# Kernel optimization log

Hardware: AMD Instinct MI355X
Metric: run time of the kernel (lower is better)

The kernel has to match this reference:

```python
import jax, jax.numpy as jnp
import numpy as np

C = 768      # token feature dim
N = 196      # tokens per stream
R_DIM = 2 * 2 * N  # 784 = concat(A row, A col)


def setup_inputs() -> dict:
    key = jax.random.key(0)
    ks = jax.random.split(key, 16)
    s = 1.0 / np.sqrt(C)
    inp = {
        "x": jax.random.normal(ks[0], (128, N, C), dtype=jnp.float32),
        "y": jax.random.normal(ks[1], (128, N, C), dtype=jnp.float32),
        # linear_conv_1: 1x1 conv (768->768) + BN affine (eval) + ReLU
        "W1": jax.random.normal(ks[2], (C, C), dtype=jnp.float32) * s,
        "b1": jnp.zeros((C,), dtype=jnp.float32),
        "g1": jax.random.uniform(ks[3], (C,), dtype=jnp.float32, minval=0.5, maxval=1.5),
        "be1": jax.random.normal(ks[4], (C,), dtype=jnp.float32) * 0.1,
        # linear_conv_2
        "W2": jax.random.normal(ks[5], (C, C), dtype=jnp.float32) * s,
        "b2": jnp.zeros((C,), dtype=jnp.float32),
        "g2": jax.random.uniform(ks[6], (C,), dtype=jnp.float32, minval=0.5, maxval=1.5),
        "be2": jax.random.normal(ks[7], (C,), dtype=jnp.float32) * 0.1,
        # linear_conv_3: 768->768
        "W3": jax.random.normal(ks[8], (C, C), dtype=jnp.float32) * s,
        "b3": jnp.zeros((C,), dtype=jnp.float32),
        # linear_conv_4: 784->784 over relation rows
        "W4": jax.random.normal(ks[9], (784, 784), dtype=jnp.float32) / np.sqrt(784.0),
        "b4": jnp.zeros((784,), dtype=jnp.float32),
        # linear_conv_5: (768+784)->1
        "W5": jax.random.normal(ks[10], (C + 784, 1), dtype=jnp.float32) / np.sqrt(C + 784.0),
        "b5": jnp.zeros((1,), dtype=jnp.float32),
    }
    return inp


def reference(x, y, W1, b1, g1, be1, W2, b2, g2, be2, W3, b3, W4, b4, W5, b5):
    # per-token 1x1 conv + BN(eval)->affine + ReLU
    phi_x = jax.nn.relu((x @ W1 + b1) * g1 + be1)          # [B,196,768]
    phi_y = jax.nn.relu((y @ W2 + b2) * g2 + be2)          # [B,196,768]
    cat_phi = jnp.concatenate([phi_x, phi_y], axis=1)      # [B,392,768]
    # affinity matrix A = cat_phi @ cat_phi^T
    A = jnp.einsum("bnd,bmd->bnm", cat_phi, cat_phi)       # [B,392,392]
    # R[i] = concat(A[i,:], A[:,i]) -> vectorized as [A | A^T]
    R = jnp.concatenate([A, jnp.swapaxes(A, 1, 2)], axis=2)  # [B,392,784]
    v = cat_phi @ W3 + b3                                   # [B,392,768]
    v_ = R @ W4 + b4                                        # [B,392,784]
    cat_v = jnp.concatenate([v, v_], axis=2)                # [B,392,1552]
    W = cat_v @ W5 + b5                                     # [B,392,1]
    # per-token reweighting then sum of the two streams
    out = x * W[:, :N, :] + y * W[:, N:, :]                 # [B,196,768]
    return out
```

## Files before the change

### kernel.cpp

```cpp
#include <hip/hip_runtime.h>

typedef __bf16 bf16_t;
typedef bf16_t bf16x8 __attribute__((ext_vector_type(8)));
typedef float f32x4 __attribute__((ext_vector_type(4)));
typedef unsigned short u16x8 __attribute__((ext_vector_type(8)));
typedef unsigned short u16x4 __attribute__((ext_vector_type(4)));

#define CD 768
#define NT 196
#define NB 128
#define T2 392
#define MROWS (NB*NT)

__device__ __forceinline__ unsigned short f2bf(float f){
  unsigned u = __float_as_uint(f);
  u += 0x7fffu + ((u >> 16) & 1u);
  return (unsigned short)(u >> 16);
}
__device__ __forceinline__ float bf2f(unsigned short h){
  return __uint_as_float(((unsigned)h) << 16);
}
__device__ __forceinline__ float wave_reduce(float v){
  #pragma unroll
  for (int o = 32; o > 0; o >>= 1) v += __shfl_down(v, o, 64);
  return v;
}
__device__ __forceinline__ void gload16(const unsigned short* g, unsigned short* l){
  __builtin_amdgcn_global_load_lds(
      (const __attribute__((address_space(1))) unsigned int*)g,
      (__attribute__((address_space(3))) unsigned int*)l, 16, 0, 0);
}

__global__ __launch_bounds__(256) void prep_wt(const float* __restrict__ W1,
                        const float* __restrict__ W2,
                        unsigned short* __restrict__ W1t, unsigned short* __restrict__ W2t){
  __shared__ float tile[64][65];
  const float* src = blockIdx.z ? W2 : W1;
  unsigned short* dst = blockIdx.z ? W2t : W1t;
  int k0 = blockIdx.x*64, n0 = blockIdx.y*64;
  int tid = threadIdx.x;
  #pragma unroll
  for (int e = 0; e < 16; ++e){
    int idx = e*256 + tid;
    int r = idx >> 6, c = idx & 63;
    tile[r][c] = src[(size_t)(k0+r)*CD + n0 + c];
  }
  __syncthreads();
  #pragma unroll
  for (int e = 0; e < 16; ++e){
    int idx = e*256 + tid;
    int nr = idx >> 6, kc = idx & 63;
    dst[(size_t)(n0+nr)*CD + k0 + kc] = f2bf(tile[kc][nr]);
  }
}

__global__ void prep_u(const float* __restrict__ W3, const float* __restrict__ W4,
                       const float* __restrict__ W5, const float* __restrict__ b3,
                       const float* __restrict__ b4, const float* __restrict__ b5,
                       float* __restrict__ u3, float* __restrict__ u4s, float* __restrict__ cbuf){
  int wid = (blockIdx.x*blockDim.x + threadIdx.x) >> 6;
  int lane = threadIdx.x & 63;
  const float* w5a = W5;
  const float* w5b = W5 + CD;
  float s = 0.f;
  if (wid < CD){
    const float* row = W3 + (size_t)wid*CD;
    for (int k = lane; k < CD; k += 64) s += row[k]*w5a[k];
    s = wave_reduce(s);
    if (lane == 0) u3[wid] = s;
  } else if (wid < CD + T2){
    int j = wid - CD;
    const float* r0 = W4 + (size_t)j*784;
    const float* r1 = W4 + (size_t)(j+T2)*784;
    for (int e = lane; e < 784; e += 64) s += (r0[e]+r1[e])*w5b[e];
    s = wave_reduce(s);
    if (lane == 0) u4s[j] = s;
  } else if (wid == CD + T2){
    for (int k = lane; k < CD; k += 64) s += b3[k]*w5a[k];
    for (int e = lane; e < 784; e += 64) s += b4[e]*w5b[e];
    s = wave_reduce(s);
    if (lane == 0) cbuf[0] = s + b5[0];
  }
}

__global__ void init_t(const float* __restrict__ u3, float* __restrict__ t){
  int i = blockIdx.x*256 + threadIdx.x;
  if (i < (NB+1)*CD) t[i] = (i < NB*CD) ? u3[i % CD] : 0.f;
}

__global__ __launch_bounds__(256) void cvt2(const float* __restrict__ x,
                                            const float* __restrict__ y,
                                            unsigned short* __restrict__ dst){
  const int nv = MROWS*CD/8;
  for (int id = blockIdx.x*256 + threadIdx.x; id < 2*nv; id += gridDim.x*256){
    const float* s = (id < nv) ? x : y;
    int i = (id < nv) ? id : id - nv;
    float4 a = ((const float4*)s)[i*2];
    float4 b = ((const float4*)s)[i*2+1];
    u16x8 o = { f2bf(a.x), f2bf(a.y), f2bf(a.z), f2bf(a.w),
                f2bf(b.x), f2bf(b.y), f2bf(b.z), f2bf(b.w) };
    ((u16x8*)dst)[id] = o;
  }
}

__global__ __launch_bounds__(256, 2) void phi_gemm(
    const unsigned short* __restrict__ A, const unsigned short* __restrict__ Bt,
    const float* __restrict__ bias, const float* __restrict__ gam,
    const float* __restrict__ bet, const float* __restrict__ u4c,
    unsigned short* __restrict__ phi, float* __restrict__ t)
{
  __shared__ unsigned short As[2][128*64];
  __shared__ unsigned short Bs[2][128*64];

  const int tid  = threadIdx.x;
  const int lane = tid & 63;
  const int w    = tid >> 6;
  const int wr = w >> 1, wc = w & 1;

  int orig = blockIdx.x;
  int swz  = (orig & 7)*147 + (orig >> 3);
  int bn = swz % 6;
  int bm = swz / 6;

  const int srow = lane >> 3;
  const int p    = lane & 7;
  const int g0   = (p - srow) & 7;
  const unsigned short* a0 = A  + (size_t)(bm*128 + w*32 + srow)*CD + g0*8;
  const unsigned short* b0 = Bt + (size_t)(bn*128 + w*32 + srow)*CD + g0*8;
  unsigned short* al0 = &As[0][w*2048]; unsigned short* bl0 = &Bs[0][w*2048];
  unsigned short* al1 = &As[1][w*2048]; unsigned short* bl1 = &Bs[1][w*2048];

  const int fr = lane & 15, f = lane >> 4, r7 = lane & 7;
  f32x4 acc[4][4] = {};

#define STAGE(AL, BL, KT) { const int ko = (KT)*64;         \
    _Pragma("unroll")                                       \
    for (int c = 0; c < 4; ++c){                            \
      gload16(a0 + (size_t)c*8*CD + ko, AL + c*512);        \
      gload16(b0 + (size_t)c*8*CD + ko, BL + c*512); } }

#define COMPUTE(D) {                                                     \
    _Pragma("unroll")                                                    \
    for (int kk = 0; kk < 2; ++kk){                                      \
      bf16x8 af[4], bq[4];                                               \
      _Pragma("unroll")                                                  \
      for (int mi = 0; mi < 4; ++mi){ int rr = wr*64 + mi*16 + fr;       \
        af[mi] = *(const bf16x8*)(&As[D][rr*64 + (((kk*4+f)+r7)&7)*8]); }\
      _Pragma("unroll")                                                  \
      for (int ni = 0; ni < 4; ++ni){ int cc = wc*64 + ni*16 + fr;       \
        bq[ni] = *(const bf16x8*)(&Bs[D][cc*64 + (((kk*4+f)+r7)&7)*8]); }\
      _Pragma("unroll")                                                  \
      for (int mi = 0; mi < 4; ++mi)                                     \
        _Pragma("unroll")                                                \
        for (int ni = 0; ni < 4; ++ni)                                   \
          acc[mi][ni] = __builtin_amdgcn_mfma_f32_16x16x32_bf16(af[mi], bq[ni], acc[mi][ni], 0, 0, 0); } }

  STAGE(al0, bl0, 0)
  __syncthreads();
  #pragma unroll 1
  for (int kp = 0; kp < 5; ++kp){
    STAGE(al1, bl1, 2*kp+1)
    COMPUTE(0)
    __syncthreads();
    STAGE(al0, bl0, 2*kp+2)
    COMPUTE(1)
    __syncthreads();
  }
  STAGE(al1, bl1, 11)
  COMPUTE(0)
  __syncthreads();
  COMPUTE(1)
#undef COMPUTE
#undef STAGE

  const int b_base = (bm*128) / NT;
  #pragma unroll
  for (int ni = 0; ni < 4; ++ni){
    int col = bn*128 + wc*64 + ni*16 + fr;
    float bi = bias[col], ga = gam[col], be = bet[col];
    float c0 = 0.f, c1 = 0.f;
    #pragma unroll
    for (int mi = 0; mi < 4; ++mi){
      int r0 = bm*128 + wr*64 + mi*16 + f*4;
      #pragma unroll
      for (int j = 0; j < 4; ++j){
        int r = r0 + j;
        float v = fmaxf((acc[mi][ni][j] + bi)*ga + be, 0.f);
        phi[(size_t)r*CD + col] = f2bf(v);
        int b = r / NT;
        int tok = r - b*NT;
        float pv = u4c[tok]*v;
        if (b == b_base) c0 += pv; else c1 += pv;
      }
    }
    c0 += __shfl_xor(c0, 16, 64); c0 += __shfl_xor(c0, 32, 64);
    c1 += __shfl_xor(c1, 16, 64); c1 += __shfl_xor(c1, 32, 64);
    if (lane < 16){
      atomicAdd(&t[(size_t)b_base*CD + col], c0);
      atomicAdd(&t[(size_t)(b_base+1)*CD + col], c1);
    }
  }
}

__global__ __launch_bounds__(256) void comp_wout(
    const unsigned short* __restrict__ phiX, const unsigned short* __restrict__ phiY,
    const float* __restrict__ t, const float* __restrict__ cbuf,
    const float* __restrict__ x, const float* __restrict__ y, float* __restrict__ out)
{
  int gw   = (blockIdx.x*256 + threadIdx.x) >> 6;
  int lane = threadIdx.x & 63;
  int b = gw / NT;
  const unsigned short* px = phiX + (size_t)gw*CD;
  const unsigned short* py = phiY + (size_t)gw*CD;
  const float* tb = t + (size_t)b*CD;
  float s1 = 0.f, s2 = 0.f;
  #pragma unroll
  for (int it = 0; it < 3; ++it){
    int k = it*256 + lane*4;
    float4 tv = *(const float4*)(tb + k);
    u16x4 ux = *(const u16x4*)(px + k);
    u16x4 uy = *(const u16x4*)(py + k);
    s1 += bf2f(ux.x)*tv.x + bf2f(ux.y)*tv.y + bf2f(ux.z)*tv.z + bf2f(ux.w)*tv.w;
    s2 += bf2f(uy.x)*tv.x + bf2f(uy.y)*tv.y + bf2f(uy.z)*tv.z + bf2f(uy.w)*tv.w;
  }
  s1 = wave_reduce(s1);
  s2 = wave_reduce(s2);
  float c = cbuf[0];
  float wx = __shfl(s1, 0, 64) + c;
  float wy = __shfl(s2, 0, 64) + c;
  const float* xr = x + (size_t)gw*CD;
  const float* yr = y + (size_t)gw*CD;
  float* orow = out + (size_t)gw*CD;
  #pragma unroll
  for (int it = 0; it < 3; ++it){
    int k = it*256 + lane*4;
    float4 xv = *(const float4*)(xr + k);
    float4 yv = *(const float4*)(yr + k);
    float4 o;
    o.x = xv.x*wx + yv.x*wy;
    o.y = xv.y*wx + yv.y*wy;
    o.z = xv.z*wx + yv.z*wy;
    o.w = xv.w*wx + yv.w*wy;
    *(float4*)(orow + k) = o;
  }
}

extern "C" void kernel_launch(void* const* d_in, const int* in_sizes, int n_in,
                              void* d_out, int out_size, void* d_ws, size_t ws_size,
                              hipStream_t stream){
  const float* x  = (const float*)d_in[0];
  const float* y  = (const float*)d_in[1];
  const float* W1 = (const float*)d_in[2];
  const float* b1 = (const float*)d_in[3];
  const float* g1 = (const float*)d_in[4];
  const float* be1= (const float*)d_in[5];
  const float* W2 = (const float*)d_in[6];
  const float* b2 = (const float*)d_in[7];
  const float* g2 = (const float*)d_in[8];
  const float* be2= (const float*)d_in[9];
  const float* W3 = (const float*)d_in[10];
  const float* b3 = (const float*)d_in[11];
  const float* W4 = (const float*)d_in[12];
  const float* b4 = (const float*)d_in[13];
  const float* W5 = (const float*)d_in[14];
  const float* b5 = (const float*)d_in[15];
  float* out = (float*)d_out;

  unsigned short* W1t = (unsigned short*)d_ws;
  unsigned short* W2t = W1t + CD*CD;
  unsigned short* S0  = W2t + CD*CD;
  unsigned short* S2  = S0 + (size_t)MROWS*CD;
  unsigned short* S1  = S2 + (size_t)MROWS*CD;
  float* u3   = (float*)(S1 + (size_t)MROWS*CD);
  float* u4s  = u3 + CD;
  float* cbuf = u4s + T2;
  float* t    = cbuf + 4;

  prep_wt<<<dim3(12,12,2), 256, 0, stream>>>(W1, W2, W1t, W2t);
  prep_u<<<(CD + T2 + 4)/4, 256, 0, stream>>>(W3, W4, W5, b3, b4, b5, u3, u4s, cbuf);
  init_t<<<((NB+1)*CD + 255)/256, 256, 0, stream>>>(u3, t);

  cvt2<<<2048, 256, 0, stream>>>(x, y, S0);

  phi_gemm<<<1176, 256, 0, stream>>>(S0, W1t, b1, g1, be1, u4s,      S1, t);
  phi_gemm<<<1176, 256, 0, stream>>>(S2, W2t, b2, g2, be2, u4s + NT, S0, t);

  comp_wout<<<MROWS/4, 256, 0, stream>>>(S1, S0, t, cbuf, x, y, out);
}
```

Measured before the change: 215.6 us.

## Make phi GEMM persistent with cross-tile prefetch and read bf16 inputs in output pass

```diff
diff --git a/kernel.cpp b/kernel.cpp
--- a/kernel.cpp
+++ b/kernel.cpp
@@ -109,35 +109,33 @@
     const float* __restrict__ bet, const float* __restrict__ u4c,
     unsigned short* __restrict__ phi, float* __restrict__ t)
 {
-  __shared__ unsigned short As[2][128*64];
-  __shared__ unsigned short Bs[2][128*64];
+  __shared__ unsigned short As[2][8192];
+  __shared__ unsigned short Bs[2][8192];
 
   const int tid  = threadIdx.x;
   const int lane = tid & 63;
   const int w    = tid >> 6;
   const int wr = w >> 1, wc = w & 1;
 
-  int orig = blockIdx.x;
-  int swz  = (orig & 7)*147 + (orig >> 3);
-  int bn = swz % 6;
-  int bm = swz / 6;
-
   const int srow = lane >> 3;
   const int p    = lane & 7;
   const int g0   = (p - srow) & 7;
-  const unsigned short* a0 = A  + (size_t)(bm*128 + w*32 + srow)*CD + g0*8;
-  const unsigned short* b0 = Bt + (size_t)(bn*128 + w*32 + srow)*CD + g0*8;
-  unsigned short* al0 = &As[0][w*2048]; unsigned short* bl0 = &Bs[0][w*2048];
-  unsigned short* al1 = &As[1][w*2048]; unsigned short* bl1 = &Bs[1][w*2048];
-
+  const size_t arow = (size_t)(w*32 + srow)*CD + g0*8;
   const int fr = lane & 15, f = lane >> 4, r7 = lane & 7;
-  f32x4 acc[4][4] = {};
-
-#define STAGE(AL, BL, KT) { const int ko = (KT)*64;         \
-    _Pragma("unroll")                                       \
-    for (int c = 0; c < 4; ++c){                            \
-      gload16(a0 + (size_t)c*8*CD + ko, AL + c*512);        \
-      gload16(b0 + (size_t)c*8*CD + ko, BL + c*512); } }
+
+  const int x   = blockIdx.x & 7;
+  const int idx = blockIdx.x >> 3;
+  int c  = idx;
+  int g  = x*147 + c;
+  int bm = g/6, bn = g - 6*(g/6);
+  const unsigned short* aP = A  + (size_t)bm*128*CD + arow;
+  const unsigned short* bP = Bt + (size_t)bn*128*CD + arow;
+
+#define STAGE(D, AG, BG, KT) { const int ko = (KT)*64;                  \
+    _Pragma("unroll")                                                   \
+    for (int cc = 0; cc < 4; ++cc){                                     \
+      gload16(AG + (size_t)cc*8*CD + ko, &As[D][w*2048 + cc*512]);      \
+      gload16(BG + (size_t)cc*8*CD + ko, &Bs[D][w*2048 + cc*512]); } }
 
 #define COMPUTE(D) {                                                     \
     _Pragma("unroll")                                                    \
@@ -147,65 +145,100 @@
       for (int mi = 0; mi < 4; ++mi){ int rr = wr*64 + mi*16 + fr;       \
         af[mi] = *(const bf16x8*)(&As[D][rr*64 + (((kk*4+f)+r7)&7)*8]); }\
       _Pragma("unroll")                                                  \
-      for (int ni = 0; ni < 4; ++ni){ int cc = wc*64 + ni*16 + fr;       \
-        bq[ni] = *(const bf16x8*)(&Bs[D][cc*64 + (((kk*4+f)+r7)&7)*8]); }\
+      for (int ni = 0; ni < 4; ++ni){ int cc2 = wc*64 + ni*16 + fr;      \
+        bq[ni] = *(const bf16x8*)(&Bs[D][cc2*64 + (((kk*4+f)+r7)&7)*8]); }\
       _Pragma("unroll")                                                  \
       for (int mi = 0; mi < 4; ++mi)                                     \
         _Pragma("unroll")                                                \
         for (int ni = 0; ni < 4; ++ni)                                   \
           acc[mi][ni] = __builtin_amdgcn_mfma_f32_16x16x32_bf16(af[mi], bq[ni], acc[mi][ni], 0, 0, 0); } }
 
-  STAGE(al0, bl0, 0)
-  __syncthreads();
+#define WAIT8 asm volatile("s_waitcnt vmcnt(8)" ::: "memory")
+#define WAIT0 asm volatile("s_waitcnt vmcnt(0)" ::: "memory")
+
+  STAGE(0, aP, bP, 0)
   #pragma unroll 1
-  for (int kp = 0; kp < 5; ++kp){
-    STAGE(al1, bl1, 2*kp+1)
-    COMPUTE(0)
-    __syncthreads();
-    STAGE(al0, bl0, 2*kp+2)
-    COMPUTE(1)
-    __syncthreads();
-  }
-  STAGE(al1, bl1, 11)
-  COMPUTE(0)
-  __syncthreads();
-  COMPUTE(1)
+  while (true){
+    const int c2 = c + 64;
+    const bool hn = (c2 < 147);
+    int bm2 = 0, bn2 = 0;
+    const unsigned short *aN = aP, *bN = bP;
+    if (hn){
+      int g2 = x*147 + c2;
+      bm2 = g2/6; bn2 = g2 - 6*bm2;
+      aN = A  + (size_t)bm2*128*CD + arow;
+      bN = Bt + (size_t)bn2*128*CD + arow;
+    }
+
+    f32x4 acc[4][4];
+    #pragma unroll
+    for (int mi = 0; mi < 4; ++mi)
+      #pragma unroll
+      for (int ni = 0; ni < 4; ++ni)
+        acc[mi][ni] = f32x4{0.f,0.f,0.f,0.f};
+
+    #pragma unroll
+    for (int kt = 0; kt < 12; ++kt){
+      if (kt < 11){
+        STAGE((kt+1)&1, aP, bP, kt+1)
+        WAIT8;
+      } else if (hn){
+        STAGE(0, aN, bN, 0)
+        WAIT8;
+      } else {
+        WAIT0;
+      }
+      __builtin_amdgcn_s_barrier();
+      __builtin_amdgcn_s_setprio(1);
+      COMPUTE(kt&1)
+      __builtin_amdgcn_s_setprio(0);
+      __builtin_amdgcn_s_barrier();
+    }
+
+    const int b_base = (bm*128) / NT;
+    #pragma unroll
+    for (int ni = 0; ni < 4; ++ni){
+      int col = bn*128 + wc*64 + ni*16 + fr;
+      float bi = bias[col], ga = gam[col], be = bet[col];
+      float c0 = 0.f, c1 = 0.f;
+      #pragma unroll
+      for (int mi = 0; mi < 4; ++mi){
+        int r0 = bm*128 + wr*64 + mi*16 + f*4;
+        #pragma unroll
+        for (int j = 0; j < 4; ++j){
+          int r = r0 + j;
+          float v = fmaxf((acc[mi][ni][j] + bi)*ga + be, 0.f);
+          phi[(size_t)r*CD + col] = f2bf(v);
+          int b = r / NT;
+          int tok = r - b*NT;
+          float pv = u4c[tok]*v;
+          if (b == b_base) c0 += pv; else c1 += pv;
+        }
+      }
+      c0 += __shfl_xor(c0, 16, 64); c0 += __shfl_xor(c0, 32, 64);
+      c1 += __shfl_xor(c1, 16, 64); c1 += __shfl_xor(c1, 32, 64);
+      if (lane < 16){
+        atomicAdd(&t[(size_t)b_base*CD + col], c0);
+        atomicAdd(&t[(size_t)(b_base+1)*CD + col], c1);
+      }
+    }
+
+    if (!hn) break;
+    c = c2; bm = bm2; bn = bn2; aP = aN; bP = bN;
+  }
+#undef WAIT0
+#undef WAIT8
 #undef COMPUTE
 #undef STAGE
-
-  const int b_base = (bm*128) / NT;
-  #pragma unroll
-  for (int ni = 0; ni < 4; ++ni){
-    int col = bn*128 + wc*64 + ni*16 + fr;
-    float bi = bias[col], ga = gam[col], be = bet[col];
-    float c0 = 0.f, c1 = 0.f;
-    #pragma unroll
-    for (int mi = 0; mi < 4; ++mi){
-      int r0 = bm*128 + wr*64 + mi*16 + f*4;
-      #pragma unroll
-      for (int j = 0; j < 4; ++j){
-        int r = r0 + j;
-        float v = fmaxf((acc[mi][ni][j] + bi)*ga + be, 0.f);
-        phi[(size_t)r*CD + col] = f2bf(v);
-        int b = r / NT;
-        int tok = r - b*NT;
-        float pv = u4c[tok]*v;
-        if (b == b_base) c0 += pv; else c1 += pv;
-      }
-    }
-    c0 += __shfl_xor(c0, 16, 64); c0 += __shfl_xor(c0, 32, 64);
-    c1 += __shfl_xor(c1, 16, 64); c1 += __shfl_xor(c1, 32, 64);
-    if (lane < 16){
-      atomicAdd(&t[(size_t)b_base*CD + col], c0);
-      atomicAdd(&t[(size_t)(b_base+1)*CD + col], c1);
-    }
-  }
-}
-
+}
+
+template<bool USEBF>
 __global__ __launch_bounds__(256) void comp_wout(
     const unsigned short* __restrict__ phiX, const unsigned short* __restrict__ phiY,
     const float* __restrict__ t, const float* __restrict__ cbuf,
-    const float* __restrict__ x, const float* __restrict__ y, float* __restrict__ out)
+    const float* __restrict__ x, const float* __restrict__ y,
+    const unsigned short* __restrict__ xb, const unsigned short* __restrict__ yb,
+    float* __restrict__ out)
 {
   int gw   = (blockIdx.x*256 + threadIdx.x) >> 6;
   int lane = threadIdx.x & 63;
@@ -225,17 +258,23 @@
   }
   s1 = wave_reduce(s1);
   s2 = wave_reduce(s2);
-  float c = cbuf[0];
-  float wx = __shfl(s1, 0, 64) + c;
-  float wy = __shfl(s2, 0, 64) + c;
-  const float* xr = x + (size_t)gw*CD;
-  const float* yr = y + (size_t)gw*CD;
+  float cc = cbuf[0];
+  float wx = __shfl(s1, 0, 64) + cc;
+  float wy = __shfl(s2, 0, 64) + cc;
   float* orow = out + (size_t)gw*CD;
   #pragma unroll
   for (int it = 0; it < 3; ++it){
     int k = it*256 + lane*4;
-    float4 xv = *(const float4*)(xr + k);
-    float4 yv = *(const float4*)(yr + k);
+    float4 xv, yv;
+    if (USEBF){
+      u16x4 a = *(const u16x4*)(xb + (size_t)gw*CD + k);
+      u16x4 c4 = *(const u16x4*)(yb + (size_t)gw*CD + k);
+      xv = float4{bf2f(a.x), bf2f(a.y), bf2f(a.z), bf2f(a.w)};
+      yv = float4{bf2f(c4.x), bf2f(c4.y), bf2f(c4.z), bf2f(c4.w)};
+    } else {
+      xv = *(const float4*)(x + (size_t)gw*CD + k);
+      yv = *(const float4*)(y + (size_t)gw*CD + k);
+    }
     float4 o;
     o.x = xv.x*wx + yv.x*wy;
     o.y = xv.y*wx + yv.y*wy;
@@ -266,12 +305,27 @@
   const float* b5 = (const float*)d_in[15];
   float* out = (float*)d_out;
 
+  const size_t BIGE = (size_t)MROWS*CD;
+  const size_t smallF = CD + T2 + 4 + (size_t)(NB+1)*CD;
+  const size_t need4 = (2*(size_t)CD*CD + 4*BIGE)*2 + smallF*4 + 256;
+  const bool big = (ws_size >= need4);
+
   unsigned short* W1t = (unsigned short*)d_ws;
   unsigned short* W2t = W1t + CD*CD;
-  unsigned short* S0  = W2t + CD*CD;
-  unsigned short* S2  = S0 + (size_t)MROWS*CD;
-  unsigned short* S1  = S2 + (size_t)MROWS*CD;
-  float* u3   = (float*)(S1 + (size_t)MROWS*CD);
+  unsigned short* Sx  = W2t + CD*CD;
+  unsigned short* Sy  = Sx + BIGE;
+  unsigned short* Px, * Py;
+  float* smalls;
+  if (big){
+    Px = Sy + BIGE;
+    Py = Px + BIGE;
+    smalls = (float*)(Py + BIGE);
+  } else {
+    Px = Sy + BIGE;
+    Py = Sx;
+    smalls = (float*)(Px + BIGE);
+  }
+  float* u3   = smalls;
   float* u4s  = u3 + CD;
   float* cbuf = u4s + T2;
   float* t    = cbuf + 4;
@@ -280,10 +334,13 @@
   prep_u<<<(CD + T2 + 4)/4, 256, 0, stream>>>(W3, W4, W5, b3, b4, b5, u3, u4s, cbuf);
   init_t<<<((NB+1)*CD + 255)/256, 256, 0, stream>>>(u3, t);
 
-  cvt2<<<2048, 256, 0, stream>>>(x, y, S0);
-
-  phi_gemm<<<1176, 256, 0, stream>>>(S0, W1t, b1, g1, be1, u4s,      S1, t);
-  phi_gemm<<<1176, 256, 0, stream>>>(S2, W2t, b2, g2, be2, u4s + NT, S0, t);
-
-  comp_wout<<<MROWS/4, 256, 0, stream>>>(S1, S0, t, cbuf, x, y, out);
-}
+  cvt2<<<2048, 256, 0, stream>>>(x, y, Sx);
+
+  phi_gemm<<<512, 256, 0, stream>>>(Sx, W1t, b1, g1, be1, u4s,      Px, t);
+  phi_gemm<<<512, 256, 0, stream>>>(Sy, W2t, b2, g2, be2, u4s + NT, Py, t);
+
+  if (big)
+    comp_wout<true><<<MROWS/4, 256, 0, stream>>>(Px, Py, t, cbuf, x, y, Sx, Sy, out);
+  else
+    comp_wout<false><<<MROWS/4, 256, 0, stream>>>(Px, Py, t, cbuf, x, y, Sx, Sy, out);
+}
```

Measured after the change: 231.0 us. 1.07x slower.
